# Kernel tuning notes

Measured on AMD Instinct MI355X. Metric: run time of the kernel, lower is better.

## Reference

```python
import jax, jax.numpy as jnp
import numpy as np

B, N, C = 8, 2048, 1024
SPARSITY = 0.8
K_KEEP = int(N * SPARSITY)  # 1638
NEG = 1e10


def setup_inputs() -> dict:
    key = jax.random.key(0)
    ks = jax.random.split(key, 7)
    s = 1.0 / np.sqrt(C)
    return {
        "x": jax.random.normal(ks[0], (B, N, C), dtype=jnp.float32),
        "Wq": jax.random.uniform(ks[1], (C, C), dtype=jnp.float32, minval=-s, maxval=s),
        "bq": jax.random.uniform(ks[2], (C,), dtype=jnp.float32, minval=-s, maxval=s),
        "Wk": jax.random.uniform(ks[3], (C, C), dtype=jnp.float32, minval=-s, maxval=s),
        "bk": jax.random.uniform(ks[4], (C,), dtype=jnp.float32, minval=-s, maxval=s),
        "Wv": jax.random.uniform(ks[5], (C, C), dtype=jnp.float32, minval=-s, maxval=s),
        "bv": jax.random.uniform(ks[6], (C,), dtype=jnp.float32, minval=-s, maxval=s),
    }


def reference(x, Wq, bq, Wk, bk, Wv, bv):
    # Linear projections (torch Linear: y = x @ W.T + b)
    Q = jnp.einsum("bnc,dc->bnd", x, Wq) + bq
    Kt = jnp.einsum("bnc,dc->bnd", x, Wk) + bk
    V = jnp.einsum("bnc,dc->bnd", x, Wv) + bv
    attn = jnp.einsum("bnd,bmd->bnm", Q, Kt) / jnp.sqrt(jnp.float32(C))  # [B,N,N]
    _, idx = jax.lax.top_k(attn, K_KEEP)  # idx: [B,N,K_KEEP]
    bI = jnp.arange(B)[:, None, None]
    nI = jnp.arange(N)[None, :, None]
    mask = jnp.zeros_like(attn).at[bI, nI, idx].set(1.0)
    attn = attn * mask - NEG * (1.0 - mask)
    attn = jax.nn.softmax(attn, axis=-1)
    return jnp.einsum("bnm,bmd->bnd", attn, V)
```

## Files before the change

### kernel.cpp

```cpp
#include <hip/hip_runtime.h>

typedef _Float16 f16;
typedef __attribute__((ext_vector_type(8))) _Float16 f16x8;
typedef __attribute__((ext_vector_type(4))) _Float16 f16x4;
typedef __attribute__((ext_vector_type(4))) float f32x4;

constexpr int BB = 8;
constexpr int NN = 2048;
constexpr int CC = 1024;
constexpr int MTOT = BB * NN;
constexpr int KKEEP = 1638;

__device__ __forceinline__ void gl_lds16(const void* g, void* l) {
  __builtin_amdgcn_global_load_lds((__attribute__((address_space(1))) void*)g,
                                   (__attribute__((address_space(3))) void*)l,
                                   16, 0, 0);
}

__global__ __launch_bounds__(256) void cvt_f32_f16(const float* __restrict__ s,
                                                   f16* __restrict__ d, int n4) {
  int i = blockIdx.x * 256 + threadIdx.x;
  if (i < n4) {
    float4 f = ((const float4*)s)[i];
    f16x4 o = {(f16)f.x, (f16)f.y, (f16)f.z, (f16)f.w};
    ((f16x4*)d)[i] = o;
  }
}

template <int MODE>
__global__ __launch_bounds__(256, 2) void gemm_bt(
    const f16* __restrict__ A, const f16* __restrict__ B,
    const float* __restrict__ bias, void* __restrict__ Cout,
    int K, int lda, int ldb, int ldc, float scale, int ldct,
    long strideA, long strideB, long strideC) {
  const f16* Ab = A + (size_t)blockIdx.z * strideA;
  const f16* Bbp = B + (size_t)blockIdx.z * strideB;

  const int bm = blockIdx.x * 128;
  const int bn = blockIdx.y * 128;
  const int tid = threadIdx.x;
  const int wave = tid >> 6;
  const int lane = tid & 63;
  const int wy = wave >> 1, wx = wave & 1;

  __shared__ f16 As[128 * 32];
  __shared__ f16 Bs[128 * 32];

  f32x4 acc[4][4];
#pragma unroll
  for (int i = 0; i < 4; i++)
#pragma unroll
    for (int j = 0; j < 4; j++) acc[i][j] = (f32x4){0.f, 0.f, 0.f, 0.f};

  const int sr = wave * 32 + (lane >> 2);
  const int sc = (lane & 3) * 8;
  const f16* gA0 = Ab + (size_t)(bm + sr) * lda + sc;
  const f16* gA1 = gA0 + (size_t)16 * lda;
  const f16* gB0 = Bbp + (size_t)(bn + sr) * ldb + sc;
  const f16* gB1 = gB0 + (size_t)16 * ldb;
  f16* lA0 = As + (wave * 32) * 32;
  f16* lA1 = As + (wave * 32 + 16) * 32;
  f16* lB0 = Bs + (wave * 32) * 32;
  f16* lB1 = Bs + (wave * 32 + 16) * 32;

  const int frm = wy * 64 + (lane & 15);
  const int frn = wx * 64 + (lane & 15);
  const int kq = (lane >> 4) * 8;

  for (int k0 = 0; k0 < K; k0 += 32) {
    gl_lds16(gA0 + k0, lA0);
    gl_lds16(gA1 + k0, lA1);
    gl_lds16(gB0 + k0, lB0);
    gl_lds16(gB1 + k0, lB1);
    __syncthreads();
    f16x8 av[4], bv[4];
#pragma unroll
    for (int i = 0; i < 4; i++)
      av[i] = *(const f16x8*)(As + (frm + 16 * i) * 32 + kq);
#pragma unroll
    for (int i = 0; i < 4; i++)
      bv[i] = *(const f16x8*)(Bs + (frn + 16 * i) * 32 + kq);
#pragma unroll
    for (int i = 0; i < 4; i++)
#pragma unroll
      for (int j = 0; j < 4; j++)
        acc[i][j] =
            __builtin_amdgcn_mfma_f32_16x16x32_f16(av[i], bv[j], acc[i][j], 0, 0, 0);
    __syncthreads();
  }

  const int q = lane >> 4;
  const int ci = lane & 15;
#pragma unroll
  for (int i = 0; i < 4; i++) {
#pragma unroll
    for (int j = 0; j < 4; j++) {
      const int row0 = bm + wy * 64 + i * 16 + q * 4;
      const int col = bn + wx * 64 + j * 16 + ci;
      if (MODE == 0) {
        float* C = (float*)Cout + (size_t)blockIdx.z * strideC;
#pragma unroll
        for (int r = 0; r < 4; r++)
          C[(size_t)(row0 + r) * ldc + col] = acc[i][j][r] * scale;
      } else if (MODE == 1) {
        f16* C = (f16*)Cout + (size_t)blockIdx.z * strideC;
        const float bb = bias[col];
#pragma unroll
        for (int r = 0; r < 4; r++)
          C[(size_t)(row0 + r) * ldc + col] = (f16)(acc[i][j][r] + bb);
      } else {
        f16* C = (f16*)Cout;
        const float bb = bias[col];
        f16x4 o;
#pragma unroll
        for (int r = 0; r < 4; r++) o[r] = (f16)(acc[i][j][r] + bb);
        *(f16x4*)(C + (size_t)col * ldct + row0) = o;
      }
    }
  }
}

__global__ __launch_bounds__(256) void topk_softmax_kernel(
    const float* __restrict__ S, f16* __restrict__ P) {
  const size_t row = blockIdx.x;
  const float* srow = S + row * 2048;
  f16* prow = P + row * 2048;
  const int t = threadIdx.x;
  const int lane = t & 63;
  const int wave = t >> 6;

  float v[8];
  float4 f0 = ((const float4*)srow)[2 * t];
  float4 f1 = ((const float4*)srow)[2 * t + 1];
  v[0] = f0.x; v[1] = f0.y; v[2] = f0.z; v[3] = f0.w;
  v[4] = f1.x; v[5] = f1.y; v[6] = f1.z; v[7] = f1.w;

  __shared__ float wlo[4], whi[4];
  __shared__ float wf[4];
  __shared__ int wagg[4];
  __shared__ int hist[2048];
  __shared__ float cval[128];
  __shared__ int cidx[128];
  __shared__ int cnum;
  __shared__ int sh_thr, sh_want;

  float lo = v[0], hi = v[0];
#pragma unroll
  for (int j = 1; j < 8; j++) { lo = fminf(lo, v[j]); hi = fmaxf(hi, v[j]); }
#pragma unroll
  for (int off = 32; off > 0; off >>= 1) {
    lo = fminf(lo, __shfl_xor(lo, off, 64));
    hi = fmaxf(hi, __shfl_xor(hi, off, 64));
  }
  if (lane == 0) { wlo[wave] = lo; whi[wave] = hi; }
  if (t == 0) cnum = 0;
  ((int4*)hist)[2 * t] = (int4){0, 0, 0, 0};
  ((int4*)hist)[2 * t + 1] = (int4){0, 0, 0, 0};
  __syncthreads();
  lo = fminf(fminf(wlo[0], wlo[1]), fminf(wlo[2], wlo[3]));
  hi = fmaxf(fmaxf(whi[0], whi[1]), fmaxf(whi[2], whi[3]));

  if (hi == lo) {
    const float w = 1.0f / (float)KKEEP;
    f16x8 o;
#pragma unroll
    for (int j = 0; j < 8; j++) o[j] = (f16)((t * 8 + j < KKEEP) ? w : 0.f);
    *(f16x8*)(prow + t * 8) = o;
    return;
  }

  const float qs = 2048.0f / (hi - lo);
  int key[8];
#pragma unroll
  for (int j = 0; j < 8; j++) {
    int k = (int)((v[j] - lo) * qs);
    key[j] = (k > 2047) ? 2047 : k;
  }
#pragma unroll
  for (int j = 0; j < 8; j++) atomicAdd(&hist[key[j]], 1);
  __syncthreads();

  int4 h0 = ((const int4*)hist)[2 * t];
  int4 h1 = ((const int4*)hist)[2 * t + 1];
  int h[8] = {h0.x, h0.y, h0.z, h0.w, h1.x, h1.y, h1.z, h1.w};
  int s[8];
  s[7] = h[7];
#pragma unroll
  for (int j = 6; j >= 0; j--) s[j] = s[j + 1] + h[j];
  const int partial = s[0];
  int sfx = partial;
#pragma unroll
  for (int off = 1; off < 64; off <<= 1) {
    int o = __shfl_down(sfx, off, 64);
    sfx += (lane + off < 64) ? o : 0;
  }
  if (lane == 0) wagg[wave] = sfx;
  __syncthreads();
  int hiw = 0;
#pragma unroll
  for (int w = 0; w < 4; w++) hiw += (w > wave) ? wagg[w] : 0;
  const int base = (sfx - partial) + hiw;
#pragma unroll
  for (int j = 0; j < 8; j++) {
    const int cum = s[j] + base;
    const int above = cum - h[j];
    if (cum >= KKEEP && above < KKEEP) {
      sh_thr = 8 * t + j;
      sh_want = KKEEP - above;
    }
  }
  __syncthreads();
  const int thr = sh_thr;
  const int wantin = sh_want;

#pragma unroll
  for (int j = 0; j < 8; j++) {
    if (key[j] == thr) {
      int slot = atomicAdd(&cnum, 1);
      if (slot < 128) { cval[slot] = v[j]; cidx[slot] = t * 8 + j; }
    }
  }
  __syncthreads();
  const int n = (cnum < 128) ? cnum : 128;

  float e[8];
  float lsum = 0.f;
#pragma unroll
  for (int j = 0; j < 8; j++) {
    bool kept;
    if (key[j] > thr) {
      kept = true;
    } else if (key[j] < thr) {
      kept = false;
    } else {
      const int myidx = t * 8 + j;
      int rank = 0;
      for (int c = 0; c < n; c++) {
        const float cv = cval[c];
        rank += (cv > v[j] || (cv == v[j] && cidx[c] < myidx)) ? 1 : 0;
      }
      kept = rank < wantin;
    }
    e[j] = kept ? __expf(v[j] - hi) : 0.f;
    lsum += e[j];
  }
#pragma unroll
  for (int off = 32; off > 0; off >>= 1) lsum += __shfl_xor(lsum, off, 64);
  if (lane == 0) wf[wave] = lsum;
  __syncthreads();
  const float inv = 1.0f / (wf[0] + wf[1] + wf[2] + wf[3]);

  f16x8 o;
#pragma unroll
  for (int j = 0; j < 8; j++) o[j] = (f16)(e[j] * inv);
  *(f16x8*)(prow + t * 8) = o;
}

extern "C" void kernel_launch(void* const* d_in, const int* in_sizes, int n_in,
                              void* d_out, int out_size, void* d_ws, size_t ws_size,
                              hipStream_t stream) {
  (void)in_sizes; (void)n_in; (void)out_size; (void)ws_size;
  const float* x = (const float*)d_in[0];
  const float* Wq = (const float*)d_in[1];
  const float* bq = (const float*)d_in[2];
  const float* Wk = (const float*)d_in[3];
  const float* bk = (const float*)d_in[4];
  const float* Wv = (const float*)d_in[5];
  const float* bv = (const float*)d_in[6];
  float* out = (float*)d_out;

  char* ws = (char*)d_ws;
  f16* qb = (f16*)(ws + 0);
  f16* kb = (f16*)(ws + 33554432);
  f16* vtb = (f16*)(ws + 67108864);
  float* S = (float*)(ws + 100663296);
  f16* xb = (f16*)(ws + 100663296);
  f16* wqb = (f16*)(ws + 134217728);
  f16* wkb = (f16*)(ws + 136314880);
  f16* wvb = (f16*)(ws + 138412032);
  f16* Pc = (f16*)(ws + 0);

  cvt_f32_f16<<<(MTOT * CC / 4 + 255) / 256, 256, 0, stream>>>(x, xb, MTOT * CC / 4);
  cvt_f32_f16<<<(CC * CC / 4 + 255) / 256, 256, 0, stream>>>(Wq, wqb, CC * CC / 4);
  cvt_f32_f16<<<(CC * CC / 4 + 255) / 256, 256, 0, stream>>>(Wk, wkb, CC * CC / 4);
  cvt_f32_f16<<<(CC * CC / 4 + 255) / 256, 256, 0, stream>>>(Wv, wvb, CC * CC / 4);

  gemm_bt<1><<<dim3(MTOT / 128, CC / 128, 1), 256, 0, stream>>>(
      xb, wqb, bq, qb, CC, CC, CC, CC, 1.f, 0, 0, 0, 0);
  gemm_bt<1><<<dim3(MTOT / 128, CC / 128, 1), 256, 0, stream>>>(
      xb, wkb, bk, kb, CC, CC, CC, CC, 1.f, 0, 0, 0, 0);
  gemm_bt<2><<<dim3(MTOT / 128, CC / 128, 1), 256, 0, stream>>>(
      xb, wvb, bv, vtb, CC, CC, CC, 0, 1.f, MTOT, 0, 0, 0);

  gemm_bt<0><<<dim3(NN / 128, NN / 128, BB), 256, 0, stream>>>(
      qb, kb, nullptr, S, CC, CC, CC, NN, 1.f / 32.f, 0,
      (long)NN * CC, (long)NN * CC, (long)NN * NN);

  topk_softmax_kernel<<<MTOT, 256, 0, stream>>>(S, Pc);

  gemm_bt<0><<<dim3(NN / 128, CC / 128, BB), 256, 0, stream>>>(
      Pc, vtb, nullptr, out, NN, NN, MTOT, CC, 1.f, 0,
      (long)NN * NN, (long)NN, (long)NN * CC);
}
```

Baseline: 484.0 us.

## Fuse QKV projections into one GEMM, merge conversions, use K=64 swizzled tiles

Merges the four f32-to-f16 conversion launches into one kernel and the three projection GEMMs into a single GEMM over a concatenated 3072-wide weight. Q and K go into one interleaved buffer with row stride 2048, and V goes out transposed. The GEMM tile now loads K=64 per iteration, with an XOR swizzle on the LDS layout meant to reduce bank conflicts and halve the number of barriers. This doubles LDS use per block and adds branching in the epilogue and in the conversion kernel.

Measured after the change: 457.0 us. -5.6%, faster.

```diff
diff --git a/kernel.cpp b/kernel.cpp
--- a/kernel.cpp
+++ b/kernel.cpp
@@ -17,21 +17,30 @@
                                    16, 0, 0);
 }
 
-__global__ __launch_bounds__(256) void cvt_f32_f16(const float* __restrict__ s,
-                                                   f16* __restrict__ d, int n4) {
+constexpr int X4 = MTOT * CC / 4;
+constexpr int W4 = CC * CC / 4;
+__global__ __launch_bounds__(256) void cvt_all(
+    const float* __restrict__ x, const float* __restrict__ Wq,
+    const float* __restrict__ Wk, const float* __restrict__ Wv,
+    f16* __restrict__ xb, f16* __restrict__ wqkv) {
   int i = blockIdx.x * 256 + threadIdx.x;
-  if (i < n4) {
-    float4 f = ((const float4*)s)[i];
-    f16x4 o = {(f16)f.x, (f16)f.y, (f16)f.z, (f16)f.w};
-    ((f16x4*)d)[i] = o;
-  }
+  const float* s;
+  f16* d;
+  if (i < X4) { s = x; d = xb; }
+  else if (i < X4 + W4) { i -= X4; s = Wq; d = wqkv; }
+  else if (i < X4 + 2 * W4) { i -= X4 + W4; s = Wk; d = wqkv + CC * CC; }
+  else { i -= X4 + 2 * W4; s = Wv; d = wqkv + 2 * CC * CC; }
+  float4 f = ((const float4*)s)[i];
+  f16x4 o = {(f16)f.x, (f16)f.y, (f16)f.z, (f16)f.w};
+  ((f16x4*)d)[i] = o;
 }
 
 template <int MODE>
 __global__ __launch_bounds__(256, 2) void gemm_bt(
     const f16* __restrict__ A, const f16* __restrict__ B,
-    const float* __restrict__ bias, void* __restrict__ Cout,
-    int K, int lda, int ldb, int ldc, float scale, int ldct,
+    const float* __restrict__ b0, const float* __restrict__ b1,
+    const float* __restrict__ b2, void* __restrict__ Cout,
+    void* __restrict__ Cout2, int K, int lda, int ldb, int ldc, float scale,
     long strideA, long strideB, long strideC) {
   const f16* Ab = A + (size_t)blockIdx.z * strideA;
   const f16* Bbp = B + (size_t)blockIdx.z * strideB;
@@ -43,8 +52,8 @@
   const int lane = tid & 63;
   const int wy = wave >> 1, wx = wave & 1;
 
-  __shared__ f16 As[128 * 32];
-  __shared__ f16 Bs[128 * 32];
+  __shared__ f16 As[128 * 64];
+  __shared__ f16 Bs[128 * 64];
 
   f32x4 acc[4][4];
 #pragma unroll
@@ -52,45 +61,48 @@
 #pragma unroll
     for (int j = 0; j < 4; j++) acc[i][j] = (f32x4){0.f, 0.f, 0.f, 0.f};
 
-  const int sr = wave * 32 + (lane >> 2);
-  const int sc = (lane & 3) * 8;
-  const f16* gA0 = Ab + (size_t)(bm + sr) * lda + sc;
-  const f16* gA1 = gA0 + (size_t)16 * lda;
-  const f16* gB0 = Bbp + (size_t)(bn + sr) * ldb + sc;
-  const f16* gB1 = gB0 + (size_t)16 * ldb;
-  f16* lA0 = As + (wave * 32) * 32;
-  f16* lA1 = As + (wave * 32 + 16) * 32;
-  f16* lB0 = Bs + (wave * 32) * 32;
-  f16* lB1 = Bs + (wave * 32 + 16) * 32;
-
-  const int frm = wy * 64 + (lane & 15);
-  const int frn = wx * 64 + (lane & 15);
-  const int kq = (lane >> 4) * 8;
-
-  for (int k0 = 0; k0 < K; k0 += 32) {
-    gl_lds16(gA0 + k0, lA0);
-    gl_lds16(gA1 + k0, lA1);
-    gl_lds16(gB0 + k0, lB0);
-    gl_lds16(gB1 + k0, lB1);
+  const int sr = wave * 32 + (lane >> 3);
+  const int gsrc = ((lane & 7) ^ (((lane >> 3) & 1) << 2)) * 8;
+  const f16* gA0 = Ab + (size_t)(bm + sr) * lda + gsrc;
+  const f16* gB0 = Bbp + (size_t)(bn + sr) * ldb + gsrc;
+  f16* lA = As + (wave * 32) * 64 + lane * 8;
+  f16* lB = Bs + (wave * 32) * 64 + lane * 8;
+
+  const int id = lane & 15;
+  const int q = lane >> 4;
+  const int frm0 = wy * 64 + id;
+  const int frn0 = wx * 64 + id;
+  const int sw = (id & 1) << 2;
+  const int g0 = (q ^ sw) * 8;
+  const int g1 = ((q + 4) ^ sw) * 8;
+
+  for (int k0 = 0; k0 < K; k0 += 64) {
+#pragma unroll
+    for (int r = 0; r < 4; r++) {
+      gl_lds16(gA0 + (size_t)8 * r * lda + k0, lA + r * 512);
+      gl_lds16(gB0 + (size_t)8 * r * ldb + k0, lB + r * 512);
+    }
     __syncthreads();
-    f16x8 av[4], bv[4];
-#pragma unroll
-    for (int i = 0; i < 4; i++)
-      av[i] = *(const f16x8*)(As + (frm + 16 * i) * 32 + kq);
-#pragma unroll
-    for (int i = 0; i < 4; i++)
-      bv[i] = *(const f16x8*)(Bs + (frn + 16 * i) * 32 + kq);
-#pragma unroll
-    for (int i = 0; i < 4; i++)
-#pragma unroll
-      for (int j = 0; j < 4; j++)
-        acc[i][j] =
-            __builtin_amdgcn_mfma_f32_16x16x32_f16(av[i], bv[j], acc[i][j], 0, 0, 0);
+    f16x8 av[2][4], bv[2][4];
+#pragma unroll
+    for (int i = 0; i < 4; i++) {
+      av[0][i] = *(const f16x8*)(As + (frm0 + 16 * i) * 64 + g0);
+      av[1][i] = *(const f16x8*)(As + (frm0 + 16 * i) * 64 + g1);
+      bv[0][i] = *(const f16x8*)(Bs + (frn0 + 16 * i) * 64 + g0);
+      bv[1][i] = *(const f16x8*)(Bs + (frn0 + 16 * i) * 64 + g1);
+    }
+#pragma unroll
+    for (int kk = 0; kk < 2; kk++)
+#pragma unroll
+      for (int i = 0; i < 4; i++)
+#pragma unroll
+        for (int j = 0; j < 4; j++)
+          acc[i][j] = __builtin_amdgcn_mfma_f32_16x16x32_f16(av[kk][i], bv[kk][j],
+                                                             acc[i][j], 0, 0, 0);
     __syncthreads();
   }
 
-  const int q = lane >> 4;
-  const int ci = lane & 15;
+  const int ci = id;
 #pragma unroll
   for (int i = 0; i < 4; i++) {
 #pragma unroll
@@ -102,19 +114,22 @@
 #pragma unroll
         for (int r = 0; r < 4; r++)
           C[(size_t)(row0 + r) * ldc + col] = acc[i][j][r] * scale;
-      } else if (MODE == 1) {
-        f16* C = (f16*)Cout + (size_t)blockIdx.z * strideC;
-        const float bb = bias[col];
-#pragma unroll
-        for (int r = 0; r < 4; r++)
-          C[(size_t)(row0 + r) * ldc + col] = (f16)(acc[i][j][r] + bb);
       } else {
-        f16* C = (f16*)Cout;
-        const float bb = bias[col];
-        f16x4 o;
-#pragma unroll
-        for (int r = 0; r < 4; r++) o[r] = (f16)(acc[i][j][r] + bb);
-        *(f16x4*)(C + (size_t)col * ldct + row0) = o;
+        if (bn < 2048) {
+          f16* C = (f16*)Cout;
+          const float* bias = (bn < 1024) ? b0 : (b1 - 1024);
+          const float bb = bias[col];
+#pragma unroll
+          for (int r = 0; r < 4; r++)
+            C[(size_t)(row0 + r) * 2048 + col] = (f16)(acc[i][j][r] + bb);
+        } else {
+          f16* C = (f16*)Cout2;
+          const float bb = b2[col - 2048];
+          f16x4 o;
+#pragma unroll
+          for (int r = 0; r < 4; r++) o[r] = (f16)(acc[i][j][r] + bb);
+          *(f16x4*)(C + (size_t)(col - 2048) * MTOT + row0) = o;
+        }
       }
     }
   }
@@ -270,35 +285,25 @@
   float* out = (float*)d_out;
 
   char* ws = (char*)d_ws;
-  f16* qb = (f16*)(ws + 0);
-  f16* kb = (f16*)(ws + 33554432);
+  f16* qkb = (f16*)(ws + 0);
   f16* vtb = (f16*)(ws + 67108864);
   float* S = (float*)(ws + 100663296);
   f16* xb = (f16*)(ws + 100663296);
-  f16* wqb = (f16*)(ws + 134217728);
-  f16* wkb = (f16*)(ws + 136314880);
-  f16* wvb = (f16*)(ws + 138412032);
+  f16* wqkv = (f16*)(ws + 134217728);
   f16* Pc = (f16*)(ws + 0);
 
-  cvt_f32_f16<<<(MTOT * CC / 4 + 255) / 256, 256, 0, stream>>>(x, xb, MTOT * CC / 4);
-  cvt_f32_f16<<<(CC * CC / 4 + 255) / 256, 256, 0, stream>>>(Wq, wqb, CC * CC / 4);
-  cvt_f32_f16<<<(CC * CC / 4 + 255) / 256, 256, 0, stream>>>(Wk, wkb, CC * CC / 4);
-  cvt_f32_f16<<<(CC * CC / 4 + 255) / 256, 256, 0, stream>>>(Wv, wvb, CC * CC / 4);
-
-  gemm_bt<1><<<dim3(MTOT / 128, CC / 128, 1), 256, 0, stream>>>(
-      xb, wqb, bq, qb, CC, CC, CC, CC, 1.f, 0, 0, 0, 0);
-  gemm_bt<1><<<dim3(MTOT / 128, CC / 128, 1), 256, 0, stream>>>(
-      xb, wkb, bk, kb, CC, CC, CC, CC, 1.f, 0, 0, 0, 0);
-  gemm_bt<2><<<dim3(MTOT / 128, CC / 128, 1), 256, 0, stream>>>(
-      xb, wvb, bv, vtb, CC, CC, CC, 0, 1.f, MTOT, 0, 0, 0);
+  cvt_all<<<(X4 + 3 * W4 + 255) / 256, 256, 0, stream>>>(x, Wq, Wk, Wv, xb, wqkv);
+
+  gemm_bt<3><<<dim3(MTOT / 128, 3072 / 128, 1), 256, 0, stream>>>(
+      xb, wqkv, bq, bk, bv, qkb, vtb, CC, CC, CC, 0, 1.f, 0, 0, 0);
 
   gemm_bt<0><<<dim3(NN / 128, NN / 128, BB), 256, 0, stream>>>(
-      qb, kb, nullptr, S, CC, CC, CC, NN, 1.f / 32.f, 0,
-      (long)NN * CC, (long)NN * CC, (long)NN * NN);
+      qkb, qkb + 1024, nullptr, nullptr, nullptr, S, nullptr, CC, 2048, 2048, NN,
+      1.f / 32.f, (long)NN * 2048, (long)NN * 2048, (long)NN * NN);
 
   topk_softmax_kernel<<<MTOT, 256, 0, stream>>>(S, Pc);
 
   gemm_bt<0><<<dim3(NN / 128, CC / 128, BB), 256, 0, stream>>>(
-      Pc, vtb, nullptr, out, NN, NN, MTOT, CC, 1.f, 0,
+      Pc, vtb, nullptr, nullptr, nullptr, out, nullptr, NN, NN, MTOT, CC, 1.f,
       (long)NN * NN, (long)NN, (long)NN * CC);
 }
```
